# Kernel tuning notes

Measured on AMD Instinct MI355X. Metric: run time of the kernel, lower is better.

## Reference

```python
import jax, jax.numpy as jnp
import numpy as np

B, L_DEC, L_ENC = 4, 1024, 1024
D_MODEL, D_INNER, N_HEAD, D_K, D_V = 512, 256, 8, 64, 64
TEMP = D_K ** 0.5
EPS = 1e-6


def _layernorm(x, g, b):
    mu = jnp.mean(x, axis=-1, keepdims=True)
    var = jnp.mean(jnp.square(x - mu), axis=-1, keepdims=True)
    return (x - mu) * jax.lax.rsqrt(var + EPS) * g + b


def _mha(x_q, x_kv, Wq, Wk, Wv, Wfc, ln_g, ln_b, mask):
    # Faithful to source: only the query input is layer-normed; k/v use raw x_kv.
    resid = x_q
    qn = _layernorm(x_q, ln_g, ln_b)
    # Stacked per-head projections: Wq/Wk/Wv are [H, d_k, d_model]
    q = jnp.einsum('bld,hkd->bhlk', qn, Wq) / TEMP   # [B,H,Lq,dk]
    k = jnp.einsum('bld,hkd->bhlk', x_kv, Wk)        # [B,H,Lk,dk]
    v = jnp.einsum('bld,hkd->bhlk', x_kv, Wv)        # [B,H,Lk,dv]
    scores = jnp.einsum('bhqd,bhkd->bhqk', q, k)     # [B,H,Lq,Lk]
    if mask is not None:
        scores = jnp.where(mask[:, None, :, :] == 0, -jnp.inf, scores)
    attn = jax.nn.softmax(scores, axis=-1)
    out = jnp.einsum('bhqk,bhkd->bhqd', attn, v)     # [B,H,Lq,dv]
    Bq, H, Lq, dv = out.shape
    out = out.transpose(0, 2, 1, 3).reshape(Bq, Lq, H * dv)
    return out @ Wfc.T + resid


def _ffn(x, W1, b1, W2, b2, ln_g, ln_b):
    resid = x
    h = _layernorm(x, ln_g, ln_b)
    h = jax.nn.relu(h @ W1.T + b1) @ W2.T + b2
    return h + resid


def setup_inputs() -> dict:
    key = jax.random.key(0)
    ks = jax.random.split(key, 20)
    s = 0.02
    dec_input = jax.random.normal(ks[0], (B, L_DEC, D_MODEL), jnp.float32)
    enc_output = jax.random.normal(ks[1], (B, L_ENC, D_MODEL), jnp.float32)
    slf_attn_mask = jnp.tril(jnp.ones((1, L_DEC, L_DEC), jnp.int32))  # causal
    p = {}
    for i, pre in enumerate(['slf', 'enc']):
        base = 2 + i * 4
        p[f'{pre}_Wq'] = jax.random.normal(ks[base], (N_HEAD, D_K, D_MODEL), jnp.float32) * s
        p[f'{pre}_Wk'] = jax.random.normal(ks[base + 1], (N_HEAD, D_K, D_MODEL), jnp.float32) * s
        p[f'{pre}_Wv'] = jax.random.normal(ks[base + 2], (N_HEAD, D_V, D_MODEL), jnp.float32) * s
        p[f'{pre}_Wfc'] = jax.random.normal(ks[base + 3], (D_MODEL, N_HEAD * D_V), jnp.float32) * s
        p[f'{pre}_ln_g'] = jnp.ones((D_MODEL,), jnp.float32)
        p[f'{pre}_ln_b'] = jnp.zeros((D_MODEL,), jnp.float32)
    p['ffn_W1'] = jax.random.normal(ks[10], (D_INNER, D_MODEL), jnp.float32) * s
    p['ffn_b1'] = jnp.zeros((D_INNER,), jnp.float32)
    p['ffn_W2'] = jax.random.normal(ks[11], (D_MODEL, D_INNER), jnp.float32) * s
    p['ffn_b2'] = jnp.zeros((D_MODEL,), jnp.float32)
    p['ffn_ln_g'] = jnp.ones((D_MODEL,), jnp.float32)
    p['ffn_ln_b'] = jnp.zeros((D_MODEL,), jnp.float32)
    return {'dec_input': dec_input, 'enc_output': enc_output,
            'slf_attn_mask': slf_attn_mask, **p}


def reference(dec_input, enc_output,
              slf_Wq, slf_Wk, slf_Wv, slf_Wfc, slf_ln_g, slf_ln_b,
              enc_Wq, enc_Wk, enc_Wv, enc_Wfc, enc_ln_g, enc_ln_b,
              ffn_W1, ffn_b1, ffn_W2, ffn_b2, ffn_ln_g, ffn_ln_b,
              slf_attn_mask):
    x = _mha(dec_input, dec_input, slf_Wq, slf_Wk, slf_Wv, slf_Wfc,
             slf_ln_g, slf_ln_b, slf_attn_mask)
    x = _mha(x, enc_output, enc_Wq, enc_Wk, enc_Wv, enc_Wfc,
             enc_ln_g, enc_ln_b, None)
    x = _ffn(x, ffn_W1, ffn_b1, ffn_W2, ffn_b2, ffn_ln_g, ffn_ln_b)
    return x
```

## Files before the change

### kernel.cpp

```cpp
#include <hip/hip_runtime.h>
#include <hip/hip_bf16.h>
#include <math.h>

#define DMODEL 512
#define NHEAD  8
#define DHEAD  64

typedef __attribute__((ext_vector_type(8))) short bf16x8;
typedef __attribute__((ext_vector_type(4))) float f32x4;
typedef __attribute__((ext_vector_type(4))) short short4v;

static __device__ inline short f2bf(float f) {
    __hip_bfloat16 h = __float2bfloat16(f);
    return *reinterpret_cast<short*>(&h);
}

#define GLOAD_LDS16(gp, lp)                                                      \
    __builtin_amdgcn_global_load_lds(                                            \
        (const __attribute__((address_space(1))) unsigned int*)(gp),             \
        (__attribute__((address_space(3))) unsigned int*)(lp), 16, 0, 0)

struct PrepArgs {
    const float* src[10];
    short*       dst[10];
    int          n[10];
    const float* X;
    const float* gam;
    const float* bet;
    short*       Y;
    short*       Xd;
    const float* E;
    short*       Ed;
    int          ln_blocks;
};

__global__ __launch_bounds__(256) void prep_kernel(PrepArgs a) {
    const int bx = blockIdx.x;
    if (bx < a.ln_blocks) {
        int row = bx * 4 + (threadIdx.x >> 6);
        int tid = threadIdx.x & 63;
        const float* x = a.X + (size_t)row * DMODEL;
        float4 v0 = *(const float4*)(x + tid * 4);
        float4 v1 = *(const float4*)(x + 256 + tid * 4);
        float sum = v0.x + v0.y + v0.z + v0.w + v1.x + v1.y + v1.z + v1.w;
        float sq  = v0.x*v0.x + v0.y*v0.y + v0.z*v0.z + v0.w*v0.w
                  + v1.x*v1.x + v1.y*v1.y + v1.z*v1.z + v1.w*v1.w;
#pragma unroll
        for (int off = 1; off < 64; off <<= 1) {
            sum += __shfl_xor(sum, off);
            sq  += __shfl_xor(sq, off);
        }
        float mu  = sum * (1.0f / DMODEL);
        float var = sq * (1.0f / DMODEL) - mu * mu;
        float r   = rsqrtf(var + 1e-6f);
        float4 g1 = *(const float4*)(a.gam + tid * 4);
        float4 c1 = *(const float4*)(a.bet + tid * 4);
        float4 g2 = *(const float4*)(a.gam + 256 + tid * 4);
        float4 c2 = *(const float4*)(a.bet + 256 + tid * 4);
        short4v y1, y2;
        y1.x = f2bf((v0.x - mu) * r * g1.x + c1.x);
        y1.y = f2bf((v0.y - mu) * r * g1.y + c1.y);
        y1.z = f2bf((v0.z - mu) * r * g1.z + c1.z);
        y1.w = f2bf((v0.w - mu) * r * g1.w + c1.w);
        y2.x = f2bf((v1.x - mu) * r * g2.x + c2.x);
        y2.y = f2bf((v1.y - mu) * r * g2.y + c2.y);
        y2.z = f2bf((v1.z - mu) * r * g2.z + c2.z);
        y2.w = f2bf((v1.w - mu) * r * g2.w + c2.w);
        short* y = a.Y + (size_t)row * DMODEL;
        *(short4v*)(y + tid * 4)       = y1;
        *(short4v*)(y + 256 + tid * 4) = y2;
        short4v d1, d2;
        d1.x = f2bf(v0.x); d1.y = f2bf(v0.y); d1.z = f2bf(v0.z); d1.w = f2bf(v0.w);
        d2.x = f2bf(v1.x); d2.y = f2bf(v1.y); d2.z = f2bf(v1.z); d2.w = f2bf(v1.w);
        short* d = a.Xd + (size_t)row * DMODEL;
        *(short4v*)(d + tid * 4)       = d1;
        *(short4v*)(d + 256 + tid * 4) = d2;
        const float* e = a.E + (size_t)row * DMODEL;
        float4 ea = *(const float4*)(e + tid * 4);
        float4 eb = *(const float4*)(e + 256 + tid * 4);
        short4v e1, e2;
        e1.x = f2bf(ea.x); e1.y = f2bf(ea.y); e1.z = f2bf(ea.z); e1.w = f2bf(ea.w);
        e2.x = f2bf(eb.x); e2.y = f2bf(eb.y); e2.z = f2bf(eb.z); e2.w = f2bf(eb.w);
        short* ed = a.Ed + (size_t)row * DMODEL;
        *(short4v*)(ed + tid * 4)       = e1;
        *(short4v*)(ed + 256 + tid * 4) = e2;
    } else {
        int cb = bx - a.ln_blocks;
        int t = cb >> 7;
        int idx = ((cb & 127) * 256 + threadIdx.x) * 8;
        if (idx >= a.n[t]) return;
        const float* s = a.src[t] + idx;
        float4 p = *(const float4*)s;
        float4 q = *(const float4*)(s + 4);
        bf16x8 o;
        o[0] = f2bf(p.x); o[1] = f2bf(p.y); o[2] = f2bf(p.z); o[3] = f2bf(p.w);
        o[4] = f2bf(q.x); o[5] = f2bf(q.y); o[6] = f2bf(q.z); o[7] = f2bf(q.w);
        *(bf16x8*)(a.dst[t] + idx) = o;
    }
}

__global__ __launch_bounds__(256) void ln_kernel(const float* __restrict__ X,
                                                 const float* __restrict__ gam,
                                                 const float* __restrict__ bet,
                                                 short* __restrict__ Y) {
    int row = blockIdx.x * 4 + (threadIdx.x >> 6);
    int tid = threadIdx.x & 63;
    const float* x = X + (size_t)row * DMODEL;
    float4 a = *(const float4*)(x + tid * 4);
    float4 b = *(const float4*)(x + 256 + tid * 4);
    float sum = a.x + a.y + a.z + a.w + b.x + b.y + b.z + b.w;
    float sq  = a.x*a.x + a.y*a.y + a.z*a.z + a.w*a.w
              + b.x*b.x + b.y*b.y + b.z*b.z + b.w*b.w;
#pragma unroll
    for (int off = 1; off < 64; off <<= 1) {
        sum += __shfl_xor(sum, off);
        sq  += __shfl_xor(sq, off);
    }
    float mu  = sum * (1.0f / DMODEL);
    float var = sq * (1.0f / DMODEL) - mu * mu;
    float r   = rsqrtf(var + 1e-6f);
    float4 g1 = *(const float4*)(gam + tid * 4);
    float4 c1 = *(const float4*)(bet + tid * 4);
    float4 g2 = *(const float4*)(gam + 256 + tid * 4);
    float4 c2 = *(const float4*)(bet + 256 + tid * 4);
    short4v y1, y2;
    y1.x = f2bf((a.x - mu) * r * g1.x + c1.x);
    y1.y = f2bf((a.y - mu) * r * g1.y + c1.y);
    y1.z = f2bf((a.z - mu) * r * g1.z + c1.z);
    y1.w = f2bf((a.w - mu) * r * g1.w + c1.w);
    y2.x = f2bf((b.x - mu) * r * g2.x + c2.x);
    y2.y = f2bf((b.y - mu) * r * g2.y + c2.y);
    y2.z = f2bf((b.z - mu) * r * g2.z + c2.z);
    y2.w = f2bf((b.w - mu) * r * g2.w + c2.w);
    short* y = Y + (size_t)row * DMODEL;
    *(short4v*)(y + tid * 4)       = y1;
    *(short4v*)(y + 256 + tid * 4) = y2;
}

struct GJobs {
    const short* A[3];
    const short* W[3];
    const float* bias[3];
    const float* resid[3];
    void*        C[3];
    int M[3], N[3], K[3];
    float scale[3];
    int relu[3], obf[3], nblk[3];
};

__global__ __launch_bounds__(256) void gemm_bf16(GJobs jb) {
    __shared__ short As[2][64 * 64];
    __shared__ short Bs[2][64 * 64];

    int bid = blockIdx.x, j = 0;
    while (j < 2 && bid >= jb.nblk[j]) { bid -= jb.nblk[j]; ++j; }
    const short* __restrict__ A = jb.A[j];
    const short* __restrict__ W = jb.W[j];
    const int N = jb.N[j], K = jb.K[j];
    const int nbx = N >> 6;
    const int tn = (bid % nbx) * 64;
    const int tm = (bid / nbx) * 64;

    const int tid  = threadIdx.x;
    const int w    = tid >> 6;
    const int l    = tid & 63;
    const int lq   = l & 15;
    const int g    = l >> 4;
    const int wm   = (w >> 1) * 32;
    const int wn   = (w & 1) * 32;
    const int lrow = l >> 3;
    const int lsl  = l & 7;

    f32x4 acc[2][2];
#pragma unroll
    for (int i = 0; i < 2; ++i)
#pragma unroll
        for (int jj = 0; jj < 2; ++jj)
            acc[i][jj] = (f32x4){0.f, 0.f, 0.f, 0.f};

#define GSTAGE(buf, koff)                                                        \
    do {                                                                         \
        _Pragma("unroll")                                                        \
        for (int i_ = 0; i_ < 2; ++i_) {                                         \
            int row_ = i_ * 32 + w * 8 + lrow;                                   \
            int slot_ = lsl ^ (row_ & 7);                                        \
            GLOAD_LDS16(A + (size_t)(tm + row_) * K + (koff) + slot_ * 8,        \
                        As[buf] + i_ * 2048 + w * 512);                          \
            GLOAD_LDS16(W + (size_t)(tn + row_) * K + (koff) + slot_ * 8,        \
                        Bs[buf] + i_ * 2048 + w * 512);                          \
        }                                                                        \
    } while (0)

    GSTAGE(0, 0);
    int buf = 0;
#pragma unroll 1
    for (int k0 = 0; k0 < K; k0 += 64, buf ^= 1) {
        __syncthreads();
        if (k0 + 64 < K) GSTAGE(buf ^ 1, k0 + 64);
#pragma unroll
        for (int ks = 0; ks < 2; ++ks) {
            const int sl = ((ks * 4 + g) ^ (lq & 7)) * 8;
            bf16x8 af[2], bfv[2];
#pragma unroll
            for (int i = 0; i < 2; ++i) {
                af[i]  = *(const bf16x8*)&As[buf][(wm + i * 16 + lq) * 64 + sl];
                bfv[i] = *(const bf16x8*)&Bs[buf][(wn + i * 16 + lq) * 64 + sl];
            }
#pragma unroll
            for (int i = 0; i < 2; ++i)
#pragma unroll
                for (int jj = 0; jj < 2; ++jj)
                    acc[i][jj] = __builtin_amdgcn_mfma_f32_16x16x32_bf16(
                        af[i], bfv[jj], acc[i][jj], 0, 0, 0);
        }
    }
#undef GSTAGE

    const float* bias  = jb.bias[j];
    const float* resid = jb.resid[j];
    const float scale  = jb.scale[j];
    const int relu = jb.relu[j], obf = jb.obf[j];
#pragma unroll
    for (int i = 0; i < 2; ++i) {
#pragma unroll
        for (int r = 0; r < 4; ++r) {
            int row = tm + wm + i * 16 + g * 4 + r;
#pragma unroll
            for (int jj = 0; jj < 2; ++jj) {
                int col = tn + wn + jj * 16 + lq;
                float v = acc[i][jj][r] * scale;
                if (bias)  v += bias[col];
                if (resid) v += resid[(size_t)row * N + col];
                if (relu)  v = fmaxf(v, 0.f);
                if (obf) ((short*)jb.C[j])[(size_t)row * N + col] = f2bf(v);
                else     ((float*)jb.C[j])[(size_t)row * N + col] = v;
            }
        }
    }
}

__global__ __launch_bounds__(256) void attn_mfma_kernel(
        const short* __restrict__ Q, const short* __restrict__ K,
        const short* __restrict__ V, short* __restrict__ O,
        int Lq, int Lk, int causal, int qs, int kvs) {
    __shared__ short Kt[2][64 * 64];
    __shared__ short Vt[2][64][72];
    __shared__ short Pb[4][16][72];

    const int tid  = threadIdx.x;
    const int wave = tid >> 6;
    const int lane = tid & 63;
    const int lq   = lane & 15;
    const int g    = lane >> 4;
    const int bh   = blockIdx.y;
    const int b = bh >> 3, h = bh & 7;
    const int band = causal ? ((bh < 16) ? (int)blockIdx.x : (15 - (int)blockIdx.x))
                            : (int)blockIdx.x;
    const int qt = band * 4 + wave;
    const int q0 = qt * 16;
    const float NEG = -__builtin_inff();

    size_t qoff = (size_t)(b * Lq + q0 + lq) * qs + h * DHEAD;
    bf16x8 qf0 = *(const bf16x8*)(Q + qoff + g * 8);
    bf16x8 qf1 = *(const bf16x8*)(Q + qoff + 32 + g * 8);

    f32x4 o[4] = {{0,0,0,0},{0,0,0,0},{0,0,0,0},{0,0,0,0}};
    f32x4 lacc = {0.f, 0.f, 0.f, 0.f};

    bf16x8 ones;
    {
        short ov = (lq == 0) ? (short)0x3F80 : (short)0;
#pragma unroll
        for (int i = 0; i < 8; ++i) ones[i] = ov;
    }

    const int nkt = causal ? (band + 1) : (Lk >> 6);
    const int lrow = lane >> 3;
    const int lsl  = lane & 7;
    const int va = tid & 31;
    const int vd = (tid >> 5) * 8;

    bf16x8 vr0, vr1;
    auto stageK = [&](int kt, int bf) {
#pragma unroll
        for (int i = 0; i < 2; ++i) {
            int row = i * 32 + wave * 8 + lrow;
            int slot = lsl ^ (row & 7);
            GLOAD_LDS16(K + (size_t)(b * Lk + kt * 64 + row) * kvs + h * DHEAD + slot * 8,
                        Kt[bf] + i * 2048 + wave * 512);
        }
    };
    auto loadV = [&](int kt) {
        size_t gb = (size_t)(b * Lk + kt * 64 + 2 * va) * kvs + h * DHEAD + vd;
        vr0 = *(const bf16x8*)(V + gb);
        vr1 = *(const bf16x8*)(V + gb + kvs);
    };
    auto writeV = [&](int bf) {
#pragma unroll
        for (int i = 0; i < 8; ++i) {
            unsigned p = (unsigned short)vr0[i] | ((unsigned)(unsigned short)vr1[i] << 16);
            *(unsigned*)&Vt[bf][vd + i][2 * va] = p;
        }
    };

    stageK(0, 0);
    loadV(0);
    writeV(0);
    __syncthreads();

#pragma unroll 1
    for (int kt = 0; kt < nkt; ++kt) {
        const int cur = kt & 1;
        if (kt + 1 < nkt) { stageK(kt + 1, cur ^ 1); loadV(kt + 1); }

        f32x4 s[4];
#pragma unroll
        for (int sub = 0; sub < 4; ++sub) {
            int rr = sub * 16 + lq;
            const int sl0 = ((0 + g) ^ (lq & 7)) * 8;
            const int sl1 = ((4 + g) ^ (lq & 7)) * 8;
            bf16x8 kf0 = *(const bf16x8*)&Kt[cur][rr * 64 + sl0];
            bf16x8 kf1 = *(const bf16x8*)&Kt[cur][rr * 64 + sl1];
            f32x4 a = {0.f, 0.f, 0.f, 0.f};
            a = __builtin_amdgcn_mfma_f32_16x16x32_bf16(kf0, qf0, a, 0, 0, 0);
            a = __builtin_amdgcn_mfma_f32_16x16x32_bf16(kf1, qf1, a, 0, 0, 0);
            s[sub] = a;
        }
        if (causal && kt == nkt - 1) {
            int qg = q0 + lq;
#pragma unroll
            for (int sub = 0; sub < 4; ++sub) {
#pragma unroll
                for (int r = 0; r < 4; ++r) {
                    int kg = kt * 64 + sub * 16 + g * 4 + r;
                    if (kg > qg) s[sub][r] = NEG;
                }
            }
        }

#pragma unroll
        for (int sub = 0; sub < 4; ++sub) {
            short4v p4;
            p4.x = f2bf(exp2f(fminf(s[sub][0], 85.f)));
            p4.y = f2bf(exp2f(fminf(s[sub][1], 85.f)));
            p4.z = f2bf(exp2f(fminf(s[sub][2], 85.f)));
            p4.w = f2bf(exp2f(fminf(s[sub][3], 85.f)));
            *(short4v*)&Pb[wave][lq][sub * 16 + g * 4] = p4;
        }
        bf16x8 pf0 = *(const bf16x8*)&Pb[wave][lq][g * 8];
        bf16x8 pf1 = *(const bf16x8*)&Pb[wave][lq][32 + g * 8];

#pragma unroll
        for (int dc = 0; dc < 4; ++dc) {
            bf16x8 vf0 = *(const bf16x8*)&Vt[cur][dc * 16 + lq][g * 8];
            bf16x8 vf1 = *(const bf16x8*)&Vt[cur][dc * 16 + lq][32 + g * 8];
            o[dc] = __builtin_amdgcn_mfma_f32_16x16x32_bf16(pf0, vf0, o[dc], 0, 0, 0);
            o[dc] = __builtin_amdgcn_mfma_f32_16x16x32_bf16(pf1, vf1, o[dc], 0, 0, 0);
        }
        lacc = __builtin_amdgcn_mfma_f32_16x16x32_bf16(pf0, ones, lacc, 0, 0, 0);
        lacc = __builtin_amdgcn_mfma_f32_16x16x32_bf16(pf1, ones, lacc, 0, 0, 0);

        if (kt + 1 < nkt) writeV(cur ^ 1);
        __syncthreads();
    }

#pragma unroll
    for (int r = 0; r < 4; ++r) {
        float lr = __shfl(lacc[r], g << 4);
        float inv = 1.f / lr;
        size_t ob = (size_t)(b * Lq + q0 + g * 4 + r) * qs + h * DHEAD + lq;
        O[ob + 0]  = f2bf(o[0][r] * inv);
        O[ob + 16] = f2bf(o[1][r] * inv);
        O[ob + 32] = f2bf(o[2][r] * inv);
        O[ob + 48] = f2bf(o[3][r] * inv);
    }
}

static void launch_gemm(GJobs& jb, int njobs, hipStream_t stream) {
    int total = 0;
    for (int i = 0; i < 3; ++i) { if (i >= njobs) jb.nblk[i] = 0; total += jb.nblk[i]; }
    gemm_bf16<<<total, 256, 0, stream>>>(jb);
}

extern "C" void kernel_launch(void* const* d_in, const int* in_sizes, int n_in,
                              void* d_out, int out_size, void* d_ws, size_t ws_size,
                              hipStream_t stream) {
    const float* dec       = (const float*)d_in[0];
    const float* enc       = (const float*)d_in[1];
    const float* slf_Wq    = (const float*)d_in[3];
    const float* slf_Wk    = (const float*)d_in[4];
    const float* slf_Wv    = (const float*)d_in[5];
    const float* slf_Wfc   = (const float*)d_in[6];
    const float* slf_ln_g  = (const float*)d_in[7];
    const float* slf_ln_b  = (const float*)d_in[8];
    const float* enc_Wq    = (const float*)d_in[9];
    const float* enc_Wk    = (const float*)d_in[10];
    const float* enc_Wv    = (const float*)d_in[11];
    const float* enc_Wfc   = (const float*)d_in[12];
    const float* enc_ln_g  = (const float*)d_in[13];
    const float* enc_ln_b  = (const float*)d_in[14];
    const float* ffn_W1    = (const float*)d_in[15];
    const float* ffn_b1    = (const float*)d_in[16];
    const float* ffn_W2    = (const float*)d_in[17];
    const float* ffn_b2    = (const float*)d_in[18];
    const float* ffn_ln_g  = (const float*)d_in[19];
    const float* ffn_ln_b  = (const float*)d_in[20];
    float* out = (float*)d_out;

    const int Bb = 4, L = 1024, M = Bb * L;
    const size_t NE = (size_t)M * DMODEL;
    const int WQN = NHEAD * DHEAD * DMODEL;
    const float QSCALE = 0.125f * 1.44269504f;
    float* ws = (float*)d_ws;
    float* x1 = ws;
    float* x2 = ws + NE;
    short* kv16e = (short*)x2;
    short* sb = (short*)(ws + 2 * NE);
    short* dec16 = sb;               sb += NE;
    short* enc16 = sb;               sb += NE;
    short* qn16  = sb;               sb += NE;
    short* q16   = sb;               sb += NE;
    short* ao16  = sb;               sb += NE;
    short* kv16  = sb;               sb += 2 * NE;
    short* h16   = sb;               sb += NE / 2;
    short* wq_s  = sb;               sb += WQN;
    short* wkv_s = sb;               sb += 2 * WQN;
    short* wfc_s = sb;               sb += WQN;
    short* wq_e  = sb;               sb += WQN;
    short* wkv_e = sb;               sb += 2 * WQN;
    short* wfc_e = sb;               sb += WQN;
    short* w1_16 = sb;               sb += 256 * DMODEL;
    short* w2_16 = sb;               sb += DMODEL * 256;

    PrepArgs pa;
    pa.src[0] = slf_Wq;  pa.dst[0] = wq_s;          pa.n[0] = WQN;
    pa.src[1] = slf_Wk;  pa.dst[1] = wkv_s;         pa.n[1] = WQN;
    pa.src[2] = slf_Wv;  pa.dst[2] = wkv_s + WQN;   pa.n[2] = WQN;
    pa.src[3] = slf_Wfc; pa.dst[3] = wfc_s;         pa.n[3] = WQN;
    pa.src[4] = enc_Wq;  pa.dst[4] = wq_e;          pa.n[4] = WQN;
    pa.src[5] = enc_Wk;  pa.dst[5] = wkv_e;         pa.n[5] = WQN;
    pa.src[6] = enc_Wv;  pa.dst[6] = wkv_e + WQN;   pa.n[6] = WQN;
    pa.src[7] = enc_Wfc; pa.dst[7] = wfc_e;         pa.n[7] = WQN;
    pa.src[8] = ffn_W1;  pa.dst[8] = w1_16;         pa.n[8] = 256 * DMODEL;
    pa.src[9] = ffn_W2;  pa.dst[9] = w2_16;         pa.n[9] = DMODEL * 256;
    pa.X = dec; pa.gam = slf_ln_g; pa.bet = slf_ln_b; pa.Y = qn16;
    pa.Xd = dec16; pa.E = enc; pa.Ed = enc16;
    pa.ln_blocks = M / 4;
    prep_kernel<<<M / 4 + 10 * 128, 256, 0, stream>>>(pa);

    dim3 attn_grid(L / 64, Bb * NHEAD);
    const int NB512  = (M / 64) * (512 / 64);
    const int NB1024 = (M / 64) * (1024 / 64);
    const int NB256  = (M / 64) * (256 / 64);

    {
        GJobs jb = {};
        jb.A[0] = qn16;  jb.W[0] = wq_s;  jb.C[0] = q16;
        jb.M[0] = M; jb.N[0] = 512;  jb.K[0] = 512; jb.scale[0] = QSCALE;
        jb.obf[0] = 1; jb.nblk[0] = NB512;
        jb.A[1] = dec16; jb.W[1] = wkv_s; jb.C[1] = kv16;
        jb.M[1] = M; jb.N[1] = 1024; jb.K[1] = 512; jb.scale[1] = 1.f;
        jb.obf[1] = 1; jb.nblk[1] = NB1024;
        jb.A[2] = enc16; jb.W[2] = wkv_e; jb.C[2] = kv16e;
        jb.M[2] = M; jb.N[2] = 1024; jb.K[2] = 512; jb.scale[2] = 1.f;
        jb.obf[2] = 1; jb.nblk[2] = NB1024;
        launch_gemm(jb, 3, stream);
    }
    attn_mfma_kernel<<<attn_grid, 256, 0, stream>>>(q16, kv16, kv16 + 512, ao16,
                                                    L, L, 1, DMODEL, 1024);
    {
        GJobs jb = {};
        jb.A[0] = ao16; jb.W[0] = wfc_s; jb.resid[0] = dec; jb.C[0] = x1;
        jb.M[0] = M; jb.N[0] = 512; jb.K[0] = 512; jb.scale[0] = 1.f;
        jb.obf[0] = 0; jb.nblk[0] = NB512;
        launch_gemm(jb, 1, stream);
    }

    ln_kernel<<<M / 4, 256, 0, stream>>>(x1, enc_ln_g, enc_ln_b, qn16);
    {
        GJobs jb = {};
        jb.A[0] = qn16; jb.W[0] = wq_e; jb.C[0] = q16;
        jb.M[0] = M; jb.N[0] = 512; jb.K[0] = 512; jb.scale[0] = QSCALE;
        jb.obf[0] = 1; jb.nblk[0] = NB512;
        launch_gemm(jb, 1, stream);
    }
    attn_mfma_kernel<<<attn_grid, 256, 0, stream>>>(q16, kv16e, kv16e + 512, ao16,
                                                    L, L, 0, DMODEL, 1024);
    {
        GJobs jb = {};
        jb.A[0] = ao16; jb.W[0] = wfc_e; jb.resid[0] = x1; jb.C[0] = x2;
        jb.M[0] = M; jb.N[0] = 512; jb.K[0] = 512; jb.scale[0] = 1.f;
        jb.obf[0] = 0; jb.nblk[0] = NB512;
        launch_gemm(jb, 1, stream);
    }

    ln_kernel<<<M / 4, 256, 0, stream>>>(x2, ffn_ln_g, ffn_ln_b, qn16);
    {
        GJobs jb = {};
        jb.A[0] = qn16; jb.W[0] = w1_16; jb.bias[0] = ffn_b1; jb.C[0] = h16;
        jb.M[0] = M; jb.N[0] = 256; jb.K[0] = 512; jb.scale[0] = 1.f;
        jb.relu[0] = 1; jb.obf[0] = 1; jb.nblk[0] = NB256;
        launch_gemm(jb, 1, stream);
    }
    {
        GJobs jb = {};
        jb.A[0] = h16; jb.W[0] = w2_16; jb.bias[0] = ffn_b2; jb.resid[0] = x2;
        jb.C[0] = out;
        jb.M[0] = M; jb.N[0] = 512; jb.K[0] = 256; jb.scale[0] = 1.f;
        jb.obf[0] = 0; jb.nblk[0] = NB512;
        launch_gemm(jb, 1, stream);
    }
}
```

Measured before the change: 257.4 us.

## Split cross-attention over key halves with combine kernel; drop attention double-buffering

Cross-attention (non-causal) now runs as a split-K kernel over two halves of the key sequence, with a z-dimension in the grid. It writes unnormalized fp32 partial outputs and row sums, and a separate combine kernel adds them and normalizes to bf16. This doubles the number of blocks and shortens each block's loop, aiming for better occupancy. In exchange it adds an extra launch and an fp32 round-trip through reused workspace buffers. Both attention kernels also drop K/V double buffering in favour of single-buffered LDS with two barriers per tile, which cuts LDS use but removes load/compute overlap.

```diff
diff --git a/kernel.cpp b/kernel.cpp
--- a/kernel.cpp
+++ b/kernel.cpp
@@ -242,9 +242,9 @@
 __global__ __launch_bounds__(256) void attn_mfma_kernel(
         const short* __restrict__ Q, const short* __restrict__ K,
         const short* __restrict__ V, short* __restrict__ O,
-        int Lq, int Lk, int causal, int qs, int kvs) {
-    __shared__ short Kt[2][64 * 64];
-    __shared__ short Vt[2][64][72];
+        int Lq, int Lk, int qs, int kvs) {
+    __shared__ short Kt[64 * 64];
+    __shared__ short Vt[64][72];
     __shared__ short Pb[4][16][72];
 
     const int tid  = threadIdx.x;
@@ -254,8 +254,7 @@
     const int g    = lane >> 4;
     const int bh   = blockIdx.y;
     const int b = bh >> 3, h = bh & 7;
-    const int band = causal ? ((bh < 16) ? (int)blockIdx.x : (15 - (int)blockIdx.x))
-                            : (int)blockIdx.x;
+    const int band = (bh < 16) ? (int)blockIdx.x : (15 - (int)blockIdx.x);
     const int qt = band * 4 + wave;
     const int q0 = qt * 16;
     const float NEG = -__builtin_inff();
@@ -274,44 +273,33 @@
         for (int i = 0; i < 8; ++i) ones[i] = ov;
     }
 
-    const int nkt = causal ? (band + 1) : (Lk >> 6);
+    const int nkt = band + 1;
     const int lrow = lane >> 3;
     const int lsl  = lane & 7;
     const int va = tid & 31;
     const int vd = (tid >> 5) * 8;
 
-    bf16x8 vr0, vr1;
-    auto stageK = [&](int kt, int bf) {
+#pragma unroll 1
+    for (int kt = 0; kt < nkt; ++kt) {
+        __syncthreads();
 #pragma unroll
         for (int i = 0; i < 2; ++i) {
             int row = i * 32 + wave * 8 + lrow;
             int slot = lsl ^ (row & 7);
             GLOAD_LDS16(K + (size_t)(b * Lk + kt * 64 + row) * kvs + h * DHEAD + slot * 8,
-                        Kt[bf] + i * 2048 + wave * 512);
-        }
-    };
-    auto loadV = [&](int kt) {
-        size_t gb = (size_t)(b * Lk + kt * 64 + 2 * va) * kvs + h * DHEAD + vd;
-        vr0 = *(const bf16x8*)(V + gb);
-        vr1 = *(const bf16x8*)(V + gb + kvs);
-    };
-    auto writeV = [&](int bf) {
-#pragma unroll
-        for (int i = 0; i < 8; ++i) {
-            unsigned p = (unsigned short)vr0[i] | ((unsigned)(unsigned short)vr1[i] << 16);
-            *(unsigned*)&Vt[bf][vd + i][2 * va] = p;
-        }
-    };
-
-    stageK(0, 0);
-    loadV(0);
-    writeV(0);
-    __syncthreads();
-
-#pragma unroll 1
-    for (int kt = 0; kt < nkt; ++kt) {
-        const int cur = kt & 1;
-        if (kt + 1 < nkt) { stageK(kt + 1, cur ^ 1); loadV(kt + 1); }
+                        Kt + i * 2048 + wave * 512);
+        }
+        {
+            size_t gb = (size_t)(b * Lk + kt * 64 + 2 * va) * kvs + h * DHEAD + vd;
+            bf16x8 v0 = *(const bf16x8*)(V + gb);
+            bf16x8 v1 = *(const bf16x8*)(V + gb + kvs);
+#pragma unroll
+            for (int i = 0; i < 8; ++i) {
+                unsigned p = (unsigned short)v0[i] | ((unsigned)(unsigned short)v1[i] << 16);
+                *(unsigned*)&Vt[vd + i][2 * va] = p;
+            }
+        }
+        __syncthreads();
 
         f32x4 s[4];
 #pragma unroll
@@ -319,14 +307,14 @@
             int rr = sub * 16 + lq;
             const int sl0 = ((0 + g) ^ (lq & 7)) * 8;
             const int sl1 = ((4 + g) ^ (lq & 7)) * 8;
-            bf16x8 kf0 = *(const bf16x8*)&Kt[cur][rr * 64 + sl0];
-            bf16x8 kf1 = *(const bf16x8*)&Kt[cur][rr * 64 + sl1];
+            bf16x8 kf0 = *(const bf16x8*)&Kt[rr * 64 + sl0];
+            bf16x8 kf1 = *(const bf16x8*)&Kt[rr * 64 + sl1];
             f32x4 a = {0.f, 0.f, 0.f, 0.f};
             a = __builtin_amdgcn_mfma_f32_16x16x32_bf16(kf0, qf0, a, 0, 0, 0);
             a = __builtin_amdgcn_mfma_f32_16x16x32_bf16(kf1, qf1, a, 0, 0, 0);
             s[sub] = a;
         }
-        if (causal && kt == nkt - 1) {
+        if (kt == nkt - 1) {
             int qg = q0 + lq;
 #pragma unroll
             for (int sub = 0; sub < 4; ++sub) {
@@ -352,16 +340,13 @@
 
 #pragma unroll
         for (int dc = 0; dc < 4; ++dc) {
-            bf16x8 vf0 = *(const bf16x8*)&Vt[cur][dc * 16 + lq][g * 8];
-            bf16x8 vf1 = *(const bf16x8*)&Vt[cur][dc * 16 + lq][32 + g * 8];
+            bf16x8 vf0 = *(const bf16x8*)&Vt[dc * 16 + lq][g * 8];
+            bf16x8 vf1 = *(const bf16x8*)&Vt[dc * 16 + lq][32 + g * 8];
             o[dc] = __builtin_amdgcn_mfma_f32_16x16x32_bf16(pf0, vf0, o[dc], 0, 0, 0);
             o[dc] = __builtin_amdgcn_mfma_f32_16x16x32_bf16(pf1, vf1, o[dc], 0, 0, 0);
         }
         lacc = __builtin_amdgcn_mfma_f32_16x16x32_bf16(pf0, ones, lacc, 0, 0, 0);
         lacc = __builtin_amdgcn_mfma_f32_16x16x32_bf16(pf1, ones, lacc, 0, 0, 0);
-
-        if (kt + 1 < nkt) writeV(cur ^ 1);
-        __syncthreads();
     }
 
 #pragma unroll
@@ -374,6 +359,149 @@
         O[ob + 32] = f2bf(o[2][r] * inv);
         O[ob + 48] = f2bf(o[3][r] * inv);
     }
+}
+
+__global__ __launch_bounds__(256) void attn_split_kernel(
+        const short* __restrict__ Q, const short* __restrict__ K,
+        const short* __restrict__ V, float* __restrict__ U0,
+        float* __restrict__ U1, float* __restrict__ L0, float* __restrict__ L1,
+        int Lq, int Lk, int qs, int kvs) {
+    __shared__ short Kt[64 * 64];
+    __shared__ short Vt[64][72];
+    __shared__ short Pb[4][16][72];
+
+    const int tid  = threadIdx.x;
+    const int wave = tid >> 6;
+    const int lane = tid & 63;
+    const int lq   = lane & 15;
+    const int g    = lane >> 4;
+    const int bh   = blockIdx.y;
+    const int b = bh >> 3, h = bh & 7;
+    const int half = blockIdx.z;
+    const int qt = blockIdx.x * 4 + wave;
+    const int q0 = qt * 16;
+    float* __restrict__ U = half ? U1 : U0;
+    float* __restrict__ Ls = half ? L1 : L0;
+
+    size_t qoff = (size_t)(b * Lq + q0 + lq) * qs + h * DHEAD;
+    bf16x8 qf0 = *(const bf16x8*)(Q + qoff + g * 8);
+    bf16x8 qf1 = *(const bf16x8*)(Q + qoff + 32 + g * 8);
+
+    f32x4 o[4] = {{0,0,0,0},{0,0,0,0},{0,0,0,0},{0,0,0,0}};
+    f32x4 lacc = {0.f, 0.f, 0.f, 0.f};
+
+    bf16x8 ones;
+    {
+        short ov = (lq == 0) ? (short)0x3F80 : (short)0;
+#pragma unroll
+        for (int i = 0; i < 8; ++i) ones[i] = ov;
+    }
+
+    const int kt0 = half * (Lk >> 7);
+    const int kt1 = kt0 + (Lk >> 7);
+    const int lrow = lane >> 3;
+    const int lsl  = lane & 7;
+    const int va = tid & 31;
+    const int vd = (tid >> 5) * 8;
+
+#pragma unroll 1
+    for (int kt = kt0; kt < kt1; ++kt) {
+        __syncthreads();
+#pragma unroll
+        for (int i = 0; i < 2; ++i) {
+            int row = i * 32 + wave * 8 + lrow;
+            int slot = lsl ^ (row & 7);
+            GLOAD_LDS16(K + (size_t)(b * Lk + kt * 64 + row) * kvs + h * DHEAD + slot * 8,
+                        Kt + i * 2048 + wave * 512);
+        }
+        {
+            size_t gb = (size_t)(b * Lk + kt * 64 + 2 * va) * kvs + h * DHEAD + vd;
+            bf16x8 v0 = *(const bf16x8*)(V + gb);
+            bf16x8 v1 = *(const bf16x8*)(V + gb + kvs);
+#pragma unroll
+            for (int i = 0; i < 8; ++i) {
+                unsigned p = (unsigned short)v0[i] | ((unsigned)(unsigned short)v1[i] << 16);
+                *(unsigned*)&Vt[vd + i][2 * va] = p;
+            }
+        }
+        __syncthreads();
+
+        f32x4 s[4];
+#pragma unroll
+        for (int sub = 0; sub < 4; ++sub) {
+            int rr = sub * 16 + lq;
+            const int sl0 = ((0 + g) ^ (lq & 7)) * 8;
+            const int sl1 = ((4 + g) ^ (lq & 7)) * 8;
+            bf16x8 kf0 = *(const bf16x8*)&Kt[rr * 64 + sl0];
+            bf16x8 kf1 = *(const bf16x8*)&Kt[rr * 64 + sl1];
+            f32x4 a = {0.f, 0.f, 0.f, 0.f};
+            a = __builtin_amdgcn_mfma_f32_16x16x32_bf16(kf0, qf0, a, 0, 0, 0);
+            a = __builtin_amdgcn_mfma_f32_16x16x32_bf16(kf1, qf1, a, 0, 0, 0);
+            s[sub] = a;
+        }
+
+#pragma unroll
+        for (int sub = 0; sub < 4; ++sub) {
+            short4v p4;
+            p4.x = f2bf(exp2f(fminf(s[sub][0], 85.f)));
+            p4.y = f2bf(exp2f(fminf(s[sub][1], 85.f)));
+            p4.z = f2bf(exp2f(fminf(s[sub][2], 85.f)));
+            p4.w = f2bf(exp2f(fminf(s[sub][3], 85.f)));
+            *(short4v*)&Pb[wave][lq][sub * 16 + g * 4] = p4;
+        }
+        bf16x8 pf0 = *(const bf16x8*)&Pb[wave][lq][g * 8];
+        bf16x8 pf1 = *(const bf16x8*)&Pb[wave][lq][32 + g * 8];
+
+#pragma unroll
+        for (int dc = 0; dc < 4; ++dc) {
+            bf16x8 vf0 = *(const bf16x8*)&Vt[dc * 16 + lq][g * 8];
+            bf16x8 vf1 = *(const bf16x8*)&Vt[dc * 16 + lq][32 + g * 8];
+            o[dc] = __builtin_amdgcn_mfma_f32_16x16x32_bf16(pf0, vf0, o[dc], 0, 0, 0);
+            o[dc] = __builtin_amdgcn_mfma_f32_16x16x32_bf16(pf1, vf1, o[dc], 0, 0, 0);
+        }
+        lacc = __builtin_amdgcn_mfma_f32_16x16x32_bf16(pf0, ones, lacc, 0, 0, 0);
+        lacc = __builtin_amdgcn_mfma_f32_16x16x32_bf16(pf1, ones, lacc, 0, 0, 0);
+    }
+
+#pragma unroll
+    for (int r = 0; r < 4; ++r) {
+        float lr = __shfl(lacc[r], g << 4);
+        int row = q0 + g * 4 + r;
+        size_t ob = (size_t)(b * Lq + row) * qs + h * DHEAD + lq;
+        U[ob + 0]  = o[0][r];
+        U[ob + 16] = o[1][r];
+        U[ob + 32] = o[2][r];
+        U[ob + 48] = o[3][r];
+        if (lq == 0) Ls[(size_t)(b * NHEAD + h) * Lq + row] = lr;
+    }
+}
+
+__global__ __launch_bounds__(256) void attn_combine_kernel(
+        const float* __restrict__ U0, const float* __restrict__ U1,
+        const float* __restrict__ L0, const float* __restrict__ L1,
+        short* __restrict__ O) {
+    size_t idx = ((size_t)blockIdx.x * 256 + threadIdx.x) * 8;
+    int rowflat = (int)(idx >> 9);
+    int b = rowflat >> 10;
+    int q = rowflat & 1023;
+    int h = (int)((idx >> 6) & 7);
+    float l = L0[(size_t)(b * NHEAD + h) * 1024 + q] +
+              L1[(size_t)(b * NHEAD + h) * 1024 + q];
+    float inv = 1.f / l;
+    float4 a0 = *(const float4*)(U0 + idx);
+    float4 a1 = *(const float4*)(U0 + idx + 4);
+    float4 b0 = *(const float4*)(U1 + idx);
+    float4 b1 = *(const float4*)(U1 + idx + 4);
+    bf16x8 o;
+    o[0] = f2bf((a0.x + b0.x) * inv);
+    o[1] = f2bf((a0.y + b0.y) * inv);
+    o[2] = f2bf((a0.z + b0.z) * inv);
+    o[3] = f2bf((a0.w + b0.w) * inv);
+    o[4] = f2bf((a1.x + b1.x) * inv);
+    o[5] = f2bf((a1.y + b1.y) * inv);
+    o[6] = f2bf((a1.z + b1.z) * inv);
+    o[7] = f2bf((a1.w + b1.w) * inv);
+    *(bf16x8*)(O + idx) = o;
 }
 
 static void launch_gemm(GJobs& jb, int njobs, hipStream_t stream) {
@@ -431,6 +559,10 @@
     short* wfc_e = sb;               sb += WQN;
     short* w1_16 = sb;               sb += 256 * DMODEL;
     short* w2_16 = sb;               sb += DMODEL * 256;
+    float* l0    = (float*)sb;       sb += 2 * M;
+    float* l1    = (float*)sb;       sb += 2 * M;
+    float* u0 = (float*)kv16;
+    float* u1 = (float*)dec16;
 
     PrepArgs pa;
     pa.src[0] = slf_Wq;  pa.dst[0] = wq_s;          pa.n[0] = WQN;
@@ -449,6 +581,7 @@
     prep_kernel<<<M / 4 + 10 * 128, 256, 0, stream>>>(pa);
 
     dim3 attn_grid(L / 64, Bb * NHEAD);
+    dim3 attn2_grid(L / 64, Bb * NHEAD, 2);
     const int NB512  = (M / 64) * (512 / 64);
     const int NB1024 = (M / 64) * (1024 / 64);
     const int NB256  = (M / 64) * (256 / 64);
@@ -467,7 +600,7 @@
         launch_gemm(jb, 3, stream);
     }
     attn_mfma_kernel<<<attn_grid, 256, 0, stream>>>(q16, kv16, kv16 + 512, ao16,
-                                                    L, L, 1, DMODEL, 1024);
+                                                    L, L, DMODEL, 1024);
     {
         GJobs jb = {};
         jb.A[0] = ao16; jb.W[0] = wfc_s; jb.resid[0] = dec; jb.C[0] = x1;
@@ -484,8 +617,10 @@
         jb.obf[0] = 1; jb.nblk[0] = NB512;
         launch_gemm(jb, 1, stream);
     }
-    attn_mfma_kernel<<<attn_grid, 256, 0, stream>>>(q16, kv16e, kv16e + 512, ao16,
-                                                    L, L, 0, DMODEL, 1024);
+    attn_split_kernel<<<attn2_grid, 256, 0, stream>>>(q16, kv16e, kv16e + 512,
+                                                      u0, u1, l0, l1,
+                                                      L, L, DMODEL, 1024);
+    attn_combine_kernel<<<NE / 2048, 256, 0, stream>>>(u0, u1, l0, l1, ao16);
     {
         GJobs jb = {};
         jb.A[0] = ao16; jb.W[0] = wfc_e; jb.resid[0] = x1; jb.C[0] = x2;
```

Measured after the change: 256.6 us. No clear change (-0.3%).
